# Kernel optimization log

Measured on AMD Instinct MI355X. Metric: run time of the kernel, lower is better.

Reference implementation:

```python
import jax, jax.numpy as jnp
import numpy as np
from math import sqrt

# dims
B, H, P, N, D = 4, 8, 32, 32, 16   # batch, heads, n_patches, channels, patch_len
L = P * N                           # 1024 token positions
SEQ, PRED, WIN, E, NF = 512, 96, 10, 2, 6  # seq_len, pred_len, attention_window, e_layers, n_fore
EPS = float(np.finfo(np.float32).eps)      # torch RMSNorm default eps (finfo eps)


def setup_inputs() -> dict:
    key = jax.random.key(0)
    ks = jax.random.split(key, 8)
    return dict(
        tokens=jax.random.normal(ks[0], (B, H, L, D), jnp.float32),
        x_original=jax.random.normal(ks[1], (B, SEQ, N), jnp.float32),
        log_scales=jnp.full((E,), np.log(2.0), jnp.float32),
        attn_norm_w=jnp.ones((E, D), jnp.float32),
        conv_up_w=jax.random.normal(ks[2], (E, 2 * H, 1, 3), jnp.float32) * 0.1,
        conv_down_w=jax.random.normal(ks[3], (E, H, 2, 1), jnp.float32) * 0.1,
        ffn_norm_w=jnp.ones((E, D), jnp.float32),
        mix_w=jax.random.normal(ks[4], (1, H), jnp.float32) * 0.3,
        mix_b=jnp.zeros((1,), jnp.float32),
        fore_w=jax.random.normal(ks[5], (NF, P), jnp.float32) * 0.1,
        fore_b=jnp.zeros((NF,), jnp.float32),
    )


def _rms(x, w):
    # torch.nn.RMSNorm over last dim (patch_len)
    return x * jax.lax.rsqrt(jnp.mean(x * x, axis=-1, keepdims=True) + EPS) * w


def _mask():
    # pid repeated per-channel; True entries are masked out
    pid = jnp.repeat(jnp.arange(P), N)
    diff = pid[None, :] - pid[:, None]  # pid[key] - pid[query]
    return (diff <= 0) | (diff >= WIN)  # [L, L]


def _signed_attn(h, log_scale, mask):
    # scores: [B,H,L,L]; A = softmax(+s) - softmax(-s) with banded mask
    scores = jnp.einsum('bhld,bhmd->bhlm', h, h)
    scale = jnp.clip(jnp.exp(log_scale), 1.0, 30.0) / sqrt(D)
    pos = jnp.where(mask, -10000.0, scores)
    neg = jnp.where(mask, -10000.0, -scores)
    A = jax.nn.softmax(scale * pos, axis=-1) - jax.nn.softmax(scale * neg, axis=-1)
    return jnp.einsum('bhlm,bhmd->bhld', A, h)


def _conv_ffn(x, up_w, down_w, norm_w):
    # depthwise causal conv along patch time dim D; x: [B,H,L,D]
    r = x.transpose(0, 2, 1, 3).reshape(B * L, H, D)
    r = jnp.pad(r, ((0, 0), (0, 0), (2, 0)))  # causal left-pad (kernel_size-1)
    dn = ('NCH', 'OIH', 'NCH')
    r = jax.lax.conv_general_dilated(r, up_w, (1,), 'VALID', dimension_numbers=dn, feature_group_count=H)
    r = jax.nn.gelu(r, approximate=False)
    r = jax.lax.conv_general_dilated(r, down_w, (1,), 'VALID', dimension_numbers=dn, feature_group_count=H)
    r = r.reshape(B, L, H, D).transpose(0, 2, 1, 3)
    return _rms(x + r, norm_w)


def reference(tokens, x_original, log_scales, attn_norm_w, conv_up_w, conv_down_w,
              ffn_norm_w, mix_w, mix_b, fore_w, fore_b):
    mask = _mask()
    h = tokens
    for l in range(E):
        h = _rms(h + _signed_attn(h, log_scales[l], mask), attn_norm_w[l])
        h = _conv_ffn(h, conv_up_w[l], conv_down_w[l], ffn_norm_w[l])
    # aggregate heads -> forecast
    h = h.reshape(B, H, P, N, D).transpose(0, 3, 4, 2, 1)       # (B,N,D,P,H)
    h = jnp.einsum('bndph,h->bndp', h, mix_w[0]) + mix_b[0]      # channel_mixing
    f = jnp.einsum('bndp,fp->bndf', h, fore_w) + fore_b          # fore_projection
    f = f.reshape(B, N, D * NF)[:, :, -PRED:]                    # flatten + tail slice
    forecast = f.transpose(0, 2, 1)                              # (B,pred_len,N)
    return forecast, x_original
```

## Files before the change

kernel.cpp:

```cpp
#include <hip/hip_runtime.h>
#include <hip/hip_bf16.h>
#include <math.h>

#define BB 4
#define HH 8
#define PP 32
#define NN 32
#define DD 16
#define LL 1024
#define WINW 10
#define NFF 6
#define PREDL 96
#define SEQL 512
#define EPSF 1.1920928955078125e-07f
#define KROW 24
#define KTS 296
#define PROW 40
#define XROW 20

typedef __attribute__((ext_vector_type(8))) short bf16x8;
typedef __attribute__((ext_vector_type(4))) float f32x4;

__device__ inline short f2bs(float f) {
    __hip_bfloat16 h = __float2bfloat16(f);
    return *reinterpret_cast<short*>(&h);
}

__global__ __launch_bounds__(128) void layer_kernel(
    const float* __restrict__ hin, float* __restrict__ hout,
    const float* __restrict__ log_scales, const float* __restrict__ attn_norm,
    const float* __restrict__ up_w, const float* __restrict__ down_w,
    const float* __restrict__ ffn_norm, int layer)
{
    __shared__ short hK[9 * 32 * KROW];
    __shared__ short VT[16 * KTS];
    __shared__ short Pp[2][16 * PROW];
    __shared__ short Pn[2][16 * PROW];
    __shared__ float xls[32 * XROW];

    int blk = blockIdx.x;
    int bh  = blk >> 5;
    int hh  = bh & 7;
    int p0  = blk & 31;
    int nstage = min(9, (PP - 1) - p0);

    int tid  = threadIdx.x;
    int wid  = tid >> 6;
    int lane = tid & 63;
    int quad = lane >> 4, n16 = lane & 15;

    {
        const float4* src = (const float4*)(hin + ((size_t)bh * LL + (p0 + 1) * NN) * DD);
        if (nstage == 9) {
            #pragma unroll
            for (int k = 0; k < 9; ++k) {
                int i = tid + k * 128;
                int row = i >> 2, j = i & 3;
                float4 v = src[i];
                short s0 = f2bs(v.x), s1 = f2bs(v.y), s2 = f2bs(v.z), s3 = f2bs(v.w);
                unsigned long long u =
                      (unsigned long long)(unsigned short)s0
                    | ((unsigned long long)(unsigned short)s1 << 16)
                    | ((unsigned long long)(unsigned short)s2 << 32)
                    | ((unsigned long long)(unsigned short)s3 << 48);
                *(unsigned long long*)&hK[row * KROW + j * 4] = u;
                int d0 = j * 4;
                VT[(d0 + 0) * KTS + row] = s0;
                VT[(d0 + 1) * KTS + row] = s1;
                VT[(d0 + 2) * KTS + row] = s2;
                VT[(d0 + 3) * KTS + row] = s3;
            }
        } else {
            int nf4 = nstage * 128;
            for (int i = tid; i < nf4; i += 128) {
                int row = i >> 2, j = i & 3;
                float4 v = src[i];
                short s0 = f2bs(v.x), s1 = f2bs(v.y), s2 = f2bs(v.z), s3 = f2bs(v.w);
                unsigned long long u =
                      (unsigned long long)(unsigned short)s0
                    | ((unsigned long long)(unsigned short)s1 << 16)
                    | ((unsigned long long)(unsigned short)s2 << 32)
                    | ((unsigned long long)(unsigned short)s3 << 48);
                *(unsigned long long*)&hK[row * KROW + j * 4] = u;
                int d0 = j * 4;
                VT[(d0 + 0) * KTS + row] = s0;
                VT[(d0 + 1) * KTS + row] = s1;
                VT[(d0 + 2) * KTS + row] = s2;
                VT[(d0 + 3) * KTS + row] = s3;
            }
        }
    }

    bf16x8 Aq;
    #pragma unroll
    for (int j = 0; j < 8; ++j) Aq[j] = 0;
    if (quad < 2) {
        const float* qp = hin + ((size_t)bh * LL + p0 * NN + wid * 16 + n16) * DD + quad * 8;
        #pragma unroll
        for (int j = 0; j < 8; ++j) Aq[j] = f2bs(qp[j]);
    }
    float rs[4];
    #pragma unroll
    for (int r = 0; r < 4; ++r)
        rs[r] = hin[((size_t)bh * LL + p0 * NN + wid * 16 + quad * 4 + r) * DD + n16];

    float sc = fminf(fmaxf(__expf(log_scales[layer]), 1.0f), 30.0f) * 0.25f;

    __syncthreads();

    f32x4 Op, On;
    Op[0] = Op[1] = Op[2] = Op[3] = 0.f;
    On[0] = On[1] = On[2] = On[3] = 0.f;
    float lpp[4] = {0.f, 0.f, 0.f, 0.f}, lnn[4] = {0.f, 0.f, 0.f, 0.f};
    short* myPp = Pp[wid];
    short* myPn = Pn[wid];

    for (int c = 0; c < nstage; ++c) {
        int kb = c * 32;
        #pragma unroll
        for (int kt = 0; kt < 2; ++kt) {
            bf16x8 Bk;
            #pragma unroll
            for (int j = 0; j < 8; ++j) Bk[j] = 0;
            if (quad < 2)
                Bk = *(const bf16x8*)&hK[(kb + kt * 16 + n16) * KROW + quad * 8];
            f32x4 z; z[0] = z[1] = z[2] = z[3] = 0.f;
            f32x4 S = __builtin_amdgcn_mfma_f32_16x16x32_bf16(Aq, Bk, z, 0, 0, 0);
            #pragma unroll
            for (int r = 0; r < 4; ++r) {
                float s  = S[r];
                float ep = __expf(sc * s);
                float en = __expf(-sc * s);
                lpp[r] += ep; lnn[r] += en;
                int pr = quad * 4 + r, pc = kt * 16 + n16;
                myPp[pr * PROW + pc] = f2bs(ep);
                myPn[pr * PROW + pc] = f2bs(en);
            }
        }
        bf16x8 Bv = *(const bf16x8*)&VT[n16 * KTS + kb + quad * 8];
        bf16x8 Ap = *(const bf16x8*)&myPp[n16 * PROW + quad * 8];
        bf16x8 An = *(const bf16x8*)&myPn[n16 * PROW + quad * 8];
        Op = __builtin_amdgcn_mfma_f32_16x16x32_bf16(Ap, Bv, Op, 0, 0, 0);
        On = __builtin_amdgcn_mfma_f32_16x16x32_bf16(An, Bv, On, 0, 0, 0);
    }

    #pragma unroll
    for (int r = 0; r < 4; ++r) {
        float a = lpp[r], b = lnn[r];
        a += __shfl_xor(a, 1); a += __shfl_xor(a, 2); a += __shfl_xor(a, 4); a += __shfl_xor(a, 8);
        b += __shfl_xor(b, 1); b += __shfl_xor(b, 2); b += __shfl_xor(b, 4); b += __shfl_xor(b, 8);
        lpp[r] = a; lnn[r] = b;
    }

    #pragma unroll
    for (int r = 0; r < 4; ++r) {
        float lp = lpp[r], ln = lnn[r];
        float rl = (lp > 0.f) ? (1.0f / lp) : 0.f;
        float rn = (ln > 0.f) ? (1.0f / ln) : 0.f;
        float v  = rs[r] + Op[r] * rl - On[r] * rn;
        float ss = v * v;
        ss += __shfl_xor(ss, 1); ss += __shfl_xor(ss, 2);
        ss += __shfl_xor(ss, 4); ss += __shfl_xor(ss, 8);
        float rr = rsqrtf(ss * (1.0f / 16.0f) + EPSF);
        xls[(wid * 16 + quad * 4 + r) * XROW + n16] = v * rr * attn_norm[layer * DD + n16];
    }

    if (lane < 16) {
        int q = wid * 16 + lane;
        float x[16];
        #pragma unroll
        for (int j = 0; j < 4; ++j) {
            float4 v = *(const float4*)&xls[q * XROW + j * 4];
            x[j*4+0] = v.x; x[j*4+1] = v.y; x[j*4+2] = v.z; x[j*4+3] = v.w;
        }

        const float* uw = up_w + (size_t)(layer * 2 * HH + 2 * hh) * 3;
        float w00 = uw[0], w01 = uw[1], w02 = uw[2];
        float w10 = uw[3], w11 = uw[4], w12 = uw[5];
        const float* dw = down_w + (size_t)(layer * HH + hh) * 2;
        float dc0 = dw[0], dc1 = dw[1];

        float v[16], ss = 0.f;
        #pragma unroll
        for (int i = 0; i < 16; ++i) {
            float xm2 = (i >= 2) ? x[i - 2] : 0.f;
            float xm1 = (i >= 1) ? x[i - 1] : 0.f;
            float u0 = w00 * xm2 + w01 * xm1 + w02 * x[i];
            float u1 = w10 * xm2 + w11 * xm1 + w12 * x[i];
            float g0 = 0.5f * u0 * (1.0f + erff(u0 * 0.7071067811865475f));
            float g1 = 0.5f * u1 * (1.0f + erff(u1 * 0.7071067811865475f));
            float vv = x[i] + dc0 * g0 + dc1 * g1;
            v[i] = vv; ss += vv * vv;
        }
        float r2 = rsqrtf(ss * (1.0f / 16.0f) + EPSF);
        float* op = hout + ((size_t)bh * LL + p0 * NN + q) * DD;
        #pragma unroll
        for (int i = 0; i < 16; ++i) op[i] = v[i] * r2 * ffn_norm[layer * DD + i];
    }
}

__global__ void tail_kernel(const float* __restrict__ h, const float* __restrict__ mw_,
                            const float* __restrict__ mb_, const float* __restrict__ fw_,
                            const float* __restrict__ fb_, const float* __restrict__ x,
                            float* __restrict__ out)
{
    int t = blockIdx.x * 256 + threadIdx.x;
    if (t < BB * DD * NFF * NN) {
        int n = t & 31;
        int r = t >> 5;
        int fi = r % NFF; r /= NFF;
        int d = r & 15;
        int b = r >> 4;

        float mw[8];
        #pragma unroll
        for (int k = 0; k < 8; ++k) mw[k] = mw_[k];
        float mb = mb_[0];

        float acc = fb_[fi];
        for (int p = 0; p < PP; ++p) {
            float m = mb;
            #pragma unroll
            for (int k = 0; k < 8; ++k)
                m += h[(size_t)(((b * HH + k) * LL) + p * NN + n) * DD + d] * mw[k];
            acc += m * fw_[fi * PP + p];
        }
        out[t] = acc;
    } else {
        int u4 = t - BB * DD * NFF * NN;
        if (u4 < BB * SEQL * NN / 4) {
            const float4* x4 = (const float4*)x;
            float4* o4 = (float4*)(out + BB * PREDL * NN);
            o4[u4] = x4[u4];
        }
    }
}

static int find_by_size(const int* s, int n, int want, int occurrence) {
    int seen = 0;
    for (int i = 0; i < n; ++i)
        if (s[i] == want) { if (seen == occurrence) return i; ++seen; }
    return -1;
}

extern "C" void kernel_launch(void* const* d_in, const int* in_sizes, int n_in,
                              void* d_out, int out_size, void* d_ws, size_t ws_size,
                              hipStream_t stream) {
    int it  = find_by_size(in_sizes, n_in, 524288, 0);
    int ix  = find_by_size(in_sizes, n_in, 65536, 0);
    int ils = find_by_size(in_sizes, n_in, 2, 0);
    int ian = find_by_size(in_sizes, n_in, 32, 0);
    int icu = find_by_size(in_sizes, n_in, 96, 0);
    int icd = find_by_size(in_sizes, n_in, 32, 1);
    int ifn = find_by_size(in_sizes, n_in, 32, 2);
    int imw = find_by_size(in_sizes, n_in, 8, 0);
    int imb = find_by_size(in_sizes, n_in, 1, 0);
    int ifw = find_by_size(in_sizes, n_in, 192, 0);
    int ifb = find_by_size(in_sizes, n_in, 6, 0);
    if (it < 0 || ix < 0 || ils < 0 || ian < 0 || icu < 0 || icd < 0 ||
        ifn < 0 || imw < 0 || imb < 0 || ifw < 0 || ifb < 0) {
        it = 0; ix = 1; ils = 2; ian = 3; icu = 4; icd = 5; ifn = 6;
        imw = 7; imb = 8; ifw = 9; ifb = 10;
    }

    const float* tokens     = (const float*)d_in[it];
    const float* x_orig     = (const float*)d_in[ix];
    const float* log_scales = (const float*)d_in[ils];
    const float* attn_norm  = (const float*)d_in[ian];
    const float* up_w       = (const float*)d_in[icu];
    const float* down_w     = (const float*)d_in[icd];
    const float* ffn_norm   = (const float*)d_in[ifn];
    const float* mix_w      = (const float*)d_in[imw];
    const float* mix_b      = (const float*)d_in[imb];
    const float* fore_w     = (const float*)d_in[ifw];
    const float* fore_b     = (const float*)d_in[ifb];
    float* out = (float*)d_out;

    const size_t NH = (size_t)BB * HH * LL * DD;
    float* hA = (float*)d_ws;
    float* hB = hA + NH;

    layer_kernel<<<1024, 128, 0, stream>>>(tokens, hA, log_scales, attn_norm,
                                           up_w, down_w, ffn_norm, 0);
    layer_kernel<<<1024, 128, 0, stream>>>(hA, hB, log_scales, attn_norm,
                                           up_w, down_w, ffn_norm, 1);
    const int tail_threads = BB * DD * NFF * NN + BB * SEQL * NN / 4;
    tail_kernel<<<(tail_threads + 255) / 256, 256, 0, stream>>>(
        hB, mix_w, mix_b, fore_w, fore_b, x_orig, out);
}
```

Baseline: 132.2 us.

## Split key chunks across two wave pairs and read keys directly from global

Doubles the block to 256 threads so that two pairs of waves each process alternating key chunks of the banded attention. Partial outputs and softmax denominators from the second pair are reduced through shared memory before the epilogue. The K staging buffer is removed, and keys are loaded from global memory and converted to bf16 in registers. This adds parallelism per block and cuts LDS use, at the cost of an extra barrier, an idle epilogue for half the waves, and redundant global key loads.

After: 137.6 us. 4.1% more time.

```diff
diff --git a/kernel.cpp b/kernel.cpp
--- a/kernel.cpp
+++ b/kernel.cpp
@@ -13,7 +13,6 @@
 #define PREDL 96
 #define SEQL 512
 #define EPSF 1.1920928955078125e-07f
-#define KROW 24
 #define KTS 296
 #define PROW 40
 #define XROW 20
@@ -26,17 +25,18 @@
     return *reinterpret_cast<short*>(&h);
 }
 
-__global__ __launch_bounds__(128) void layer_kernel(
+__global__ __launch_bounds__(256) void layer_kernel(
     const float* __restrict__ hin, float* __restrict__ hout,
     const float* __restrict__ log_scales, const float* __restrict__ attn_norm,
     const float* __restrict__ up_w, const float* __restrict__ down_w,
     const float* __restrict__ ffn_norm, int layer)
 {
-    __shared__ short hK[9 * 32 * KROW];
     __shared__ short VT[16 * KTS];
-    __shared__ short Pp[2][16 * PROW];
-    __shared__ short Pn[2][16 * PROW];
+    __shared__ short Pp[4][16 * PROW];
+    __shared__ short Pn[4][16 * PROW];
     __shared__ float xls[32 * XROW];
+    __shared__ float xchg[2][64][8];
+    __shared__ float lsm[2][4][4][2];
 
     int blk = blockIdx.x;
     int bh  = blk >> 5;
@@ -46,48 +46,25 @@
 
     int tid  = threadIdx.x;
     int wid  = tid >> 6;
+    int qt   = wid & 1;
+    int ch   = wid >> 1;
     int lane = tid & 63;
     int quad = lane >> 4, n16 = lane & 15;
 
+    const float* hbase = hin + (size_t)bh * LL * DD;
+    const float* kglob = hbase + (size_t)(p0 + 1) * NN * DD;
+
     {
-        const float4* src = (const float4*)(hin + ((size_t)bh * LL + (p0 + 1) * NN) * DD);
-        if (nstage == 9) {
-            #pragma unroll
-            for (int k = 0; k < 9; ++k) {
-                int i = tid + k * 128;
-                int row = i >> 2, j = i & 3;
-                float4 v = src[i];
-                short s0 = f2bs(v.x), s1 = f2bs(v.y), s2 = f2bs(v.z), s3 = f2bs(v.w);
-                unsigned long long u =
-                      (unsigned long long)(unsigned short)s0
-                    | ((unsigned long long)(unsigned short)s1 << 16)
-                    | ((unsigned long long)(unsigned short)s2 << 32)
-                    | ((unsigned long long)(unsigned short)s3 << 48);
-                *(unsigned long long*)&hK[row * KROW + j * 4] = u;
-                int d0 = j * 4;
-                VT[(d0 + 0) * KTS + row] = s0;
-                VT[(d0 + 1) * KTS + row] = s1;
-                VT[(d0 + 2) * KTS + row] = s2;
-                VT[(d0 + 3) * KTS + row] = s3;
-            }
-        } else {
-            int nf4 = nstage * 128;
-            for (int i = tid; i < nf4; i += 128) {
-                int row = i >> 2, j = i & 3;
-                float4 v = src[i];
-                short s0 = f2bs(v.x), s1 = f2bs(v.y), s2 = f2bs(v.z), s3 = f2bs(v.w);
-                unsigned long long u =
-                      (unsigned long long)(unsigned short)s0
-                    | ((unsigned long long)(unsigned short)s1 << 16)
-                    | ((unsigned long long)(unsigned short)s2 << 32)
-                    | ((unsigned long long)(unsigned short)s3 << 48);
-                *(unsigned long long*)&hK[row * KROW + j * 4] = u;
-                int d0 = j * 4;
-                VT[(d0 + 0) * KTS + row] = s0;
-                VT[(d0 + 1) * KTS + row] = s1;
-                VT[(d0 + 2) * KTS + row] = s2;
-                VT[(d0 + 3) * KTS + row] = s3;
-            }
+        const float4* src = (const float4*)kglob;
+        int nf4 = nstage * 128;
+        for (int i = tid; i < nf4; i += 256) {
+            int row = i >> 2, j = i & 3;
+            float4 v = src[i];
+            int d0 = j * 4;
+            VT[(d0 + 0) * KTS + row] = f2bs(v.x);
+            VT[(d0 + 1) * KTS + row] = f2bs(v.y);
+            VT[(d0 + 2) * KTS + row] = f2bs(v.z);
+            VT[(d0 + 3) * KTS + row] = f2bs(v.w);
         }
     }
 
@@ -95,14 +72,14 @@
     #pragma unroll
     for (int j = 0; j < 8; ++j) Aq[j] = 0;
     if (quad < 2) {
-        const float* qp = hin + ((size_t)bh * LL + p0 * NN + wid * 16 + n16) * DD + quad * 8;
+        const float* qp = hbase + (size_t)(p0 * NN + qt * 16 + n16) * DD + quad * 8;
         #pragma unroll
         for (int j = 0; j < 8; ++j) Aq[j] = f2bs(qp[j]);
     }
     float rs[4];
     #pragma unroll
     for (int r = 0; r < 4; ++r)
-        rs[r] = hin[((size_t)bh * LL + p0 * NN + wid * 16 + quad * 4 + r) * DD + n16];
+        rs[r] = hbase[(size_t)(p0 * NN + qt * 16 + quad * 4 + r) * DD + n16];
 
     float sc = fminf(fmaxf(__expf(log_scales[layer]), 1.0f), 30.0f) * 0.25f;
 
@@ -115,15 +92,20 @@
     short* myPp = Pp[wid];
     short* myPn = Pn[wid];
 
-    for (int c = 0; c < nstage; ++c) {
+    for (int c = ch; c < nstage; c += 2) {
         int kb = c * 32;
         #pragma unroll
         for (int kt = 0; kt < 2; ++kt) {
             bf16x8 Bk;
             #pragma unroll
             for (int j = 0; j < 8; ++j) Bk[j] = 0;
-            if (quad < 2)
-                Bk = *(const bf16x8*)&hK[(kb + kt * 16 + n16) * KROW + quad * 8];
+            if (quad < 2) {
+                const float* kp = kglob + (size_t)(kb + kt * 16 + n16) * DD + quad * 8;
+                float4 v0 = *(const float4*)kp;
+                float4 v1 = *(const float4*)(kp + 4);
+                Bk[0] = f2bs(v0.x); Bk[1] = f2bs(v0.y); Bk[2] = f2bs(v0.z); Bk[3] = f2bs(v0.w);
+                Bk[4] = f2bs(v1.x); Bk[5] = f2bs(v1.y); Bk[6] = f2bs(v1.z); Bk[7] = f2bs(v1.w);
+            }
             f32x4 z; z[0] = z[1] = z[2] = z[3] = 0.f;
             f32x4 S = __builtin_amdgcn_mfma_f32_16x16x32_bf16(Aq, Bk, z, 0, 0, 0);
             #pragma unroll
@@ -152,50 +134,76 @@
         lpp[r] = a; lnn[r] = b;
     }
 
-    #pragma unroll
-    for (int r = 0; r < 4; ++r) {
-        float lp = lpp[r], ln = lnn[r];
-        float rl = (lp > 0.f) ? (1.0f / lp) : 0.f;
-        float rn = (ln > 0.f) ? (1.0f / ln) : 0.f;
-        float v  = rs[r] + Op[r] * rl - On[r] * rn;
-        float ss = v * v;
-        ss += __shfl_xor(ss, 1); ss += __shfl_xor(ss, 2);
-        ss += __shfl_xor(ss, 4); ss += __shfl_xor(ss, 8);
-        float rr = rsqrtf(ss * (1.0f / 16.0f) + EPSF);
-        xls[(wid * 16 + quad * 4 + r) * XROW + n16] = v * rr * attn_norm[layer * DD + n16];
-    }
-
-    if (lane < 16) {
-        int q = wid * 16 + lane;
-        float x[16];
-        #pragma unroll
-        for (int j = 0; j < 4; ++j) {
-            float4 v = *(const float4*)&xls[q * XROW + j * 4];
-            x[j*4+0] = v.x; x[j*4+1] = v.y; x[j*4+2] = v.z; x[j*4+3] = v.w;
-        }
-
-        const float* uw = up_w + (size_t)(layer * 2 * HH + 2 * hh) * 3;
-        float w00 = uw[0], w01 = uw[1], w02 = uw[2];
-        float w10 = uw[3], w11 = uw[4], w12 = uw[5];
-        const float* dw = down_w + (size_t)(layer * HH + hh) * 2;
-        float dc0 = dw[0], dc1 = dw[1];
-
-        float v[16], ss = 0.f;
-        #pragma unroll
-        for (int i = 0; i < 16; ++i) {
-            float xm2 = (i >= 2) ? x[i - 2] : 0.f;
-            float xm1 = (i >= 1) ? x[i - 1] : 0.f;
-            float u0 = w00 * xm2 + w01 * xm1 + w02 * x[i];
-            float u1 = w10 * xm2 + w11 * xm1 + w12 * x[i];
-            float g0 = 0.5f * u0 * (1.0f + erff(u0 * 0.7071067811865475f));
-            float g1 = 0.5f * u1 * (1.0f + erff(u1 * 0.7071067811865475f));
-            float vv = x[i] + dc0 * g0 + dc1 * g1;
-            v[i] = vv; ss += vv * vv;
-        }
-        float r2 = rsqrtf(ss * (1.0f / 16.0f) + EPSF);
-        float* op = hout + ((size_t)bh * LL + p0 * NN + q) * DD;
-        #pragma unroll
-        for (int i = 0; i < 16; ++i) op[i] = v[i] * r2 * ffn_norm[layer * DD + i];
+    if (ch == 1) {
+        #pragma unroll
+        for (int r = 0; r < 4; ++r) {
+            xchg[qt][lane][r]     = Op[r];
+            xchg[qt][lane][r + 4] = On[r];
+        }
+        if (n16 == 0) {
+            #pragma unroll
+            for (int r = 0; r < 4; ++r) {
+                lsm[qt][quad][r][0] = lpp[r];
+                lsm[qt][quad][r][1] = lnn[r];
+            }
+        }
+    }
+    __syncthreads();
+
+    if (ch == 0) {
+        #pragma unroll
+        for (int r = 0; r < 4; ++r) {
+            Op[r]  += xchg[qt][lane][r];
+            On[r]  += xchg[qt][lane][r + 4];
+            lpp[r] += lsm[qt][quad][r][0];
+            lnn[r] += lsm[qt][quad][r][1];
+        }
+
+        #pragma unroll
+        for (int r = 0; r < 4; ++r) {
+            float lp = lpp[r], ln = lnn[r];
+            float rl = (lp > 0.f) ? (1.0f / lp) : 0.f;
+            float rn = (ln > 0.f) ? (1.0f / ln) : 0.f;
+            float v  = rs[r] + Op[r] * rl - On[r] * rn;
+            float ss = v * v;
+            ss += __shfl_xor(ss, 1); ss += __shfl_xor(ss, 2);
+            ss += __shfl_xor(ss, 4); ss += __shfl_xor(ss, 8);
+            float rr = rsqrtf(ss * (1.0f / 16.0f) + EPSF);
+            xls[(qt * 16 + quad * 4 + r) * XROW + n16] = v * rr * attn_norm[layer * DD + n16];
+        }
+
+        if (lane < 16) {
+            int q = qt * 16 + lane;
+            float x[16];
+            #pragma unroll
+            for (int j = 0; j < 4; ++j) {
+                float4 v = *(const float4*)&xls[q * XROW + j * 4];
+                x[j*4+0] = v.x; x[j*4+1] = v.y; x[j*4+2] = v.z; x[j*4+3] = v.w;
+            }
+
+            const float* uw = up_w + (size_t)(layer * 2 * HH + 2 * hh) * 3;
+            float w00 = uw[0], w01 = uw[1], w02 = uw[2];
+            float w10 = uw[3], w11 = uw[4], w12 = uw[5];
+            const float* dw = down_w + (size_t)(layer * HH + hh) * 2;
+            float dc0 = dw[0], dc1 = dw[1];
+
+            float v[16], ss = 0.f;
+            #pragma unroll
+            for (int i = 0; i < 16; ++i) {
+                float xm2 = (i >= 2) ? x[i - 2] : 0.f;
+                float xm1 = (i >= 1) ? x[i - 1] : 0.f;
+                float u0 = w00 * xm2 + w01 * xm1 + w02 * x[i];
+                float u1 = w10 * xm2 + w11 * xm1 + w12 * x[i];
+                float g0 = 0.5f * u0 * (1.0f + erff(u0 * 0.7071067811865475f));
+                float g1 = 0.5f * u1 * (1.0f + erff(u1 * 0.7071067811865475f));
+                float vv = x[i] + dc0 * g0 + dc1 * g1;
+                v[i] = vv; ss += vv * vv;
+            }
+            float r2 = rsqrtf(ss * (1.0f / 16.0f) + EPSF);
+            float* op = hout + ((size_t)bh * LL + p0 * NN + q) * DD;
+            #pragma unroll
+            for (int i = 0; i < 16; ++i) op[i] = v[i] * r2 * ffn_norm[layer * DD + i];
+        }
     }
 }
 
@@ -280,9 +288,9 @@
     float* hA = (float*)d_ws;
     float* hB = hA + NH;
 
-    layer_kernel<<<1024, 128, 0, stream>>>(tokens, hA, log_scales, attn_norm,
+    layer_kernel<<<1024, 256, 0, stream>>>(tokens, hA, log_scales, attn_norm,
                                            up_w, down_w, ffn_norm, 0);
-    layer_kernel<<<1024, 128, 0, stream>>>(hA, hB, log_scales, attn_norm,
+    layer_kernel<<<1024, 256, 0, stream>>>(hA, hB, log_scales, attn_norm,
                                            up_w, down_w, ffn_norm, 1);
     const int tail_threads = BB * DD * NFF * NN + BB * SEQL * NN / 4;
     tail_kernel<<<(tail_threads + 255) / 256, 256, 0, stream>>>(
```

## Fuse both layers and tail into one cooperative kernel with grid syncs

Applied to the files above, without the earlier changes.

Merges the two layer launches and the tail launch into a single cooperative kernel of 1024 blocks, using grid-wide syncs between stages. The aim is to remove kernel launch gaps and inter-kernel drain and fill. Shared memory moves into a struct passed by pointer. If the cooperative launch fails it falls back to the old three-launch path, and grid.sync adds barrier cost.

Result: slower. 337.6 us (+155.4%).

```diff
diff --git a/kernel.cpp b/kernel.cpp
--- a/kernel.cpp
+++ b/kernel.cpp
@@ -1,6 +1,9 @@
 #include <hip/hip_runtime.h>
 #include <hip/hip_bf16.h>
+#include <hip/hip_cooperative_groups.h>
 #include <math.h>
+
+namespace cg = cooperative_groups;
 
 #define BB 4
 #define HH 8
@@ -26,18 +29,21 @@
     return *reinterpret_cast<short*>(&h);
 }
 
-__global__ __launch_bounds__(128) void layer_kernel(
+struct __align__(16) LayerSmem {
+    short hK[9 * 32 * KROW];
+    short VT[16 * KTS];
+    short Pp[2][16 * PROW];
+    short Pn[2][16 * PROW];
+    float xls[32 * XROW];
+};
+
+__device__ __forceinline__ void do_layer(
+    LayerSmem* sm,
     const float* __restrict__ hin, float* __restrict__ hout,
     const float* __restrict__ log_scales, const float* __restrict__ attn_norm,
     const float* __restrict__ up_w, const float* __restrict__ down_w,
     const float* __restrict__ ffn_norm, int layer)
 {
-    __shared__ short hK[9 * 32 * KROW];
-    __shared__ short VT[16 * KTS];
-    __shared__ short Pp[2][16 * PROW];
-    __shared__ short Pn[2][16 * PROW];
-    __shared__ float xls[32 * XROW];
-
     int blk = blockIdx.x;
     int bh  = blk >> 5;
     int hh  = bh & 7;
@@ -63,12 +69,12 @@
                     | ((unsigned long long)(unsigned short)s1 << 16)
                     | ((unsigned long long)(unsigned short)s2 << 32)
                     | ((unsigned long long)(unsigned short)s3 << 48);
-                *(unsigned long long*)&hK[row * KROW + j * 4] = u;
+                *(unsigned long long*)&sm->hK[row * KROW + j * 4] = u;
                 int d0 = j * 4;
-                VT[(d0 + 0) * KTS + row] = s0;
-                VT[(d0 + 1) * KTS + row] = s1;
-                VT[(d0 + 2) * KTS + row] = s2;
-                VT[(d0 + 3) * KTS + row] = s3;
+                sm->VT[(d0 + 0) * KTS + row] = s0;
+                sm->VT[(d0 + 1) * KTS + row] = s1;
+                sm->VT[(d0 + 2) * KTS + row] = s2;
+                sm->VT[(d0 + 3) * KTS + row] = s3;
             }
         } else {
             int nf4 = nstage * 128;
@@ -81,12 +87,12 @@
                     | ((unsigned long long)(unsigned short)s1 << 16)
                     | ((unsigned long long)(unsigned short)s2 << 32)
                     | ((unsigned long long)(unsigned short)s3 << 48);
-                *(unsigned long long*)&hK[row * KROW + j * 4] = u;
+                *(unsigned long long*)&sm->hK[row * KROW + j * 4] = u;
                 int d0 = j * 4;
-                VT[(d0 + 0) * KTS + row] = s0;
-                VT[(d0 + 1) * KTS + row] = s1;
-                VT[(d0 + 2) * KTS + row] = s2;
-                VT[(d0 + 3) * KTS + row] = s3;
+                sm->VT[(d0 + 0) * KTS + row] = s0;
+                sm->VT[(d0 + 1) * KTS + row] = s1;
+                sm->VT[(d0 + 2) * KTS + row] = s2;
+                sm->VT[(d0 + 3) * KTS + row] = s3;
             }
         }
     }
@@ -112,8 +118,8 @@
     Op[0] = Op[1] = Op[2] = Op[3] = 0.f;
     On[0] = On[1] = On[2] = On[3] = 0.f;
     float lpp[4] = {0.f, 0.f, 0.f, 0.f}, lnn[4] = {0.f, 0.f, 0.f, 0.f};
-    short* myPp = Pp[wid];
-    short* myPn = Pn[wid];
+    short* myPp = sm->Pp[wid];
+    short* myPn = sm->Pn[wid];
 
     for (int c = 0; c < nstage; ++c) {
         int kb = c * 32;
@@ -123,7 +129,7 @@
             #pragma unroll
             for (int j = 0; j < 8; ++j) Bk[j] = 0;
             if (quad < 2)
-                Bk = *(const bf16x8*)&hK[(kb + kt * 16 + n16) * KROW + quad * 8];
+                Bk = *(const bf16x8*)&sm->hK[(kb + kt * 16 + n16) * KROW + quad * 8];
             f32x4 z; z[0] = z[1] = z[2] = z[3] = 0.f;
             f32x4 S = __builtin_amdgcn_mfma_f32_16x16x32_bf16(Aq, Bk, z, 0, 0, 0);
             #pragma unroll
@@ -137,7 +143,7 @@
                 myPn[pr * PROW + pc] = f2bs(en);
             }
         }
-        bf16x8 Bv = *(const bf16x8*)&VT[n16 * KTS + kb + quad * 8];
+        bf16x8 Bv = *(const bf16x8*)&sm->VT[n16 * KTS + kb + quad * 8];
         bf16x8 Ap = *(const bf16x8*)&myPp[n16 * PROW + quad * 8];
         bf16x8 An = *(const bf16x8*)&myPn[n16 * PROW + quad * 8];
         Op = __builtin_amdgcn_mfma_f32_16x16x32_bf16(Ap, Bv, Op, 0, 0, 0);
@@ -162,7 +168,7 @@
         ss += __shfl_xor(ss, 1); ss += __shfl_xor(ss, 2);
         ss += __shfl_xor(ss, 4); ss += __shfl_xor(ss, 8);
         float rr = rsqrtf(ss * (1.0f / 16.0f) + EPSF);
-        xls[(wid * 16 + quad * 4 + r) * XROW + n16] = v * rr * attn_norm[layer * DD + n16];
+        sm->xls[(wid * 16 + quad * 4 + r) * XROW + n16] = v * rr * attn_norm[layer * DD + n16];
     }
 
     if (lane < 16) {
@@ -170,7 +176,7 @@
         float x[16];
         #pragma unroll
         for (int j = 0; j < 4; ++j) {
-            float4 v = *(const float4*)&xls[q * XROW + j * 4];
+            float4 v = *(const float4*)&sm->xls[q * XROW + j * 4];
             x[j*4+0] = v.x; x[j*4+1] = v.y; x[j*4+2] = v.z; x[j*4+3] = v.w;
         }
 
@@ -199,12 +205,12 @@
     }
 }
 
-__global__ void tail_kernel(const float* __restrict__ h, const float* __restrict__ mw_,
-                            const float* __restrict__ mb_, const float* __restrict__ fw_,
-                            const float* __restrict__ fb_, const float* __restrict__ x,
-                            float* __restrict__ out)
-{
-    int t = blockIdx.x * 256 + threadIdx.x;
+__device__ __forceinline__ void do_tail(
+    int t, const float* __restrict__ h, const float* __restrict__ mw_,
+    const float* __restrict__ mb_, const float* __restrict__ fw_,
+    const float* __restrict__ fb_, const float* __restrict__ x,
+    float* __restrict__ out)
+{
     if (t < BB * DD * NFF * NN) {
         int n = t & 31;
         int r = t >> 5;
@@ -234,6 +240,44 @@
             o4[u4] = x4[u4];
         }
     }
+}
+
+__global__ __launch_bounds__(128) void mega_kernel(
+    const float* __restrict__ tokens, float* __restrict__ hA, float* __restrict__ hB,
+    const float* __restrict__ log_scales, const float* __restrict__ attn_norm,
+    const float* __restrict__ up_w, const float* __restrict__ down_w,
+    const float* __restrict__ ffn_norm, const float* __restrict__ mw_,
+    const float* __restrict__ mb_, const float* __restrict__ fw_,
+    const float* __restrict__ fb_, const float* __restrict__ x,
+    float* __restrict__ out)
+{
+    __shared__ LayerSmem sm;
+    cg::grid_group grid = cg::this_grid();
+
+    do_layer(&sm, tokens, hA, log_scales, attn_norm, up_w, down_w, ffn_norm, 0);
+    grid.sync();
+    do_layer(&sm, hA, hB, log_scales, attn_norm, up_w, down_w, ffn_norm, 1);
+    grid.sync();
+
+    do_tail(blockIdx.x * 128 + threadIdx.x, hB, mw_, mb_, fw_, fb_, x, out);
+}
+
+__global__ __launch_bounds__(128) void layer_kernel(
+    const float* __restrict__ hin, float* __restrict__ hout,
+    const float* __restrict__ log_scales, const float* __restrict__ attn_norm,
+    const float* __restrict__ up_w, const float* __restrict__ down_w,
+    const float* __restrict__ ffn_norm, int layer)
+{
+    __shared__ LayerSmem sm;
+    do_layer(&sm, hin, hout, log_scales, attn_norm, up_w, down_w, ffn_norm, layer);
+}
+
+__global__ void tail_kernel(const float* __restrict__ h, const float* __restrict__ mw_,
+                            const float* __restrict__ mb_, const float* __restrict__ fw_,
+                            const float* __restrict__ fb_, const float* __restrict__ x,
+                            float* __restrict__ out)
+{
+    do_tail(blockIdx.x * 256 + threadIdx.x, h, mw_, mb_, fw_, fb_, x, out);
 }
 
 static int find_by_size(const int* s, int n, int want, int occurrence) {
@@ -280,11 +324,22 @@
     float* hA = (float*)d_ws;
     float* hB = hA + NH;
 
-    layer_kernel<<<1024, 128, 0, stream>>>(tokens, hA, log_scales, attn_norm,
-                                           up_w, down_w, ffn_norm, 0);
-    layer_kernel<<<1024, 128, 0, stream>>>(hA, hB, log_scales, attn_norm,
-                                           up_w, down_w, ffn_norm, 1);
-    const int tail_threads = BB * DD * NFF * NN + BB * SEQL * NN / 4;
-    tail_kernel<<<(tail_threads + 255) / 256, 256, 0, stream>>>(
-        hB, mix_w, mix_b, fore_w, fore_b, x_orig, out);
-}
+    void* args[] = {
+        (void*)&tokens, (void*)&hA, (void*)&hB, (void*)&log_scales,
+        (void*)&attn_norm, (void*)&up_w, (void*)&down_w, (void*)&ffn_norm,
+        (void*)&mix_w, (void*)&mix_b, (void*)&fore_w, (void*)&fore_b,
+        (void*)&x_orig, (void*)&out
+    };
+    hipError_t err = hipLaunchCooperativeKernel((void*)mega_kernel, dim3(1024),
+                                                dim3(128), args, 0, stream);
+    if (err != hipSuccess) {
+        (void)hipGetLastError();
+        layer_kernel<<<1024, 128, 0, stream>>>(tokens, hA, log_scales, attn_norm,
+                                               up_w, down_w, ffn_norm, 0);
+        layer_kernel<<<1024, 128, 0, stream>>>(hA, hB, log_scales, attn_norm,
+                                               up_w, down_w, ffn_norm, 1);
+        const int tail_threads = BB * DD * NFF * NN + BB * SEQL * NN / 4;
+        tail_kernel<<<(tail_threads + 255) / 256, 256, 0, stream>>>(
+            hB, mix_w, mix_b, fore_w, fore_b, x_orig, out);
+    }
+}
```

## Read K and V operands directly from global memory instead of LDS staging

Applied to the files above, without the earlier changes.

Removes the shared-memory staging of the key tile and the transposed value tile, along with the block-wide barrier that followed it. Each wave now loads its K fragments as float4 pairs and its V fragments as strided scalar loads from global memory inside the stage loop, converting them to bf16 in registers. This drops the LDS footprint and the upfront cooperative copy, which may raise occupancy. The cost is more global/L2 traffic, since both waves fetch the same keys, and uncoalesced strided V loads on the critical path of each stage.

Measured after the change: 134.9 us. 1.02x slower.

```diff
diff --git a/kernel.cpp b/kernel.cpp
--- a/kernel.cpp
+++ b/kernel.cpp
@@ -13,8 +13,6 @@
 #define PREDL 96
 #define SEQL 512
 #define EPSF 1.1920928955078125e-07f
-#define KROW 24
-#define KTS 296
 #define PROW 40
 #define XROW 20
 
@@ -32,8 +30,6 @@
     const float* __restrict__ up_w, const float* __restrict__ down_w,
     const float* __restrict__ ffn_norm, int layer)
 {
-    __shared__ short hK[9 * 32 * KROW];
-    __shared__ short VT[16 * KTS];
     __shared__ short Pp[2][16 * PROW];
     __shared__ short Pn[2][16 * PROW];
     __shared__ float xls[32 * XROW];
@@ -49,64 +45,23 @@
     int lane = tid & 63;
     int quad = lane >> 4, n16 = lane & 15;
 
-    {
-        const float4* src = (const float4*)(hin + ((size_t)bh * LL + (p0 + 1) * NN) * DD);
-        if (nstage == 9) {
-            #pragma unroll
-            for (int k = 0; k < 9; ++k) {
-                int i = tid + k * 128;
-                int row = i >> 2, j = i & 3;
-                float4 v = src[i];
-                short s0 = f2bs(v.x), s1 = f2bs(v.y), s2 = f2bs(v.z), s3 = f2bs(v.w);
-                unsigned long long u =
-                      (unsigned long long)(unsigned short)s0
-                    | ((unsigned long long)(unsigned short)s1 << 16)
-                    | ((unsigned long long)(unsigned short)s2 << 32)
-                    | ((unsigned long long)(unsigned short)s3 << 48);
-                *(unsigned long long*)&hK[row * KROW + j * 4] = u;
-                int d0 = j * 4;
-                VT[(d0 + 0) * KTS + row] = s0;
-                VT[(d0 + 1) * KTS + row] = s1;
-                VT[(d0 + 2) * KTS + row] = s2;
-                VT[(d0 + 3) * KTS + row] = s3;
-            }
-        } else {
-            int nf4 = nstage * 128;
-            for (int i = tid; i < nf4; i += 128) {
-                int row = i >> 2, j = i & 3;
-                float4 v = src[i];
-                short s0 = f2bs(v.x), s1 = f2bs(v.y), s2 = f2bs(v.z), s3 = f2bs(v.w);
-                unsigned long long u =
-                      (unsigned long long)(unsigned short)s0
-                    | ((unsigned long long)(unsigned short)s1 << 16)
-                    | ((unsigned long long)(unsigned short)s2 << 32)
-                    | ((unsigned long long)(unsigned short)s3 << 48);
-                *(unsigned long long*)&hK[row * KROW + j * 4] = u;
-                int d0 = j * 4;
-                VT[(d0 + 0) * KTS + row] = s0;
-                VT[(d0 + 1) * KTS + row] = s1;
-                VT[(d0 + 2) * KTS + row] = s2;
-                VT[(d0 + 3) * KTS + row] = s3;
-            }
-        }
-    }
+    const float* hbase = hin + (size_t)bh * LL * DD;
+    const float* kglob = hbase + (size_t)(p0 + 1) * NN * DD;
 
     bf16x8 Aq;
     #pragma unroll
     for (int j = 0; j < 8; ++j) Aq[j] = 0;
     if (quad < 2) {
-        const float* qp = hin + ((size_t)bh * LL + p0 * NN + wid * 16 + n16) * DD + quad * 8;
+        const float* qp = hbase + (size_t)(p0 * NN + wid * 16 + n16) * DD + quad * 8;
         #pragma unroll
         for (int j = 0; j < 8; ++j) Aq[j] = f2bs(qp[j]);
     }
     float rs[4];
     #pragma unroll
     for (int r = 0; r < 4; ++r)
-        rs[r] = hin[((size_t)bh * LL + p0 * NN + wid * 16 + quad * 4 + r) * DD + n16];
+        rs[r] = hbase[(size_t)(p0 * NN + wid * 16 + quad * 4 + r) * DD + n16];
 
     float sc = fminf(fmaxf(__expf(log_scales[layer]), 1.0f), 30.0f) * 0.25f;
-
-    __syncthreads();
 
     f32x4 Op, On;
     Op[0] = Op[1] = Op[2] = Op[3] = 0.f;
@@ -117,13 +72,26 @@
 
     for (int c = 0; c < nstage; ++c) {
         int kb = c * 32;
+
+        bf16x8 Bvc;
+        {
+            const float* vp = kglob + (size_t)(kb + quad * 8) * DD + n16;
+            #pragma unroll
+            for (int j = 0; j < 8; ++j) Bvc[j] = f2bs(vp[j * DD]);
+        }
+
         #pragma unroll
         for (int kt = 0; kt < 2; ++kt) {
             bf16x8 Bk;
             #pragma unroll
             for (int j = 0; j < 8; ++j) Bk[j] = 0;
-            if (quad < 2)
-                Bk = *(const bf16x8*)&hK[(kb + kt * 16 + n16) * KROW + quad * 8];
+            if (quad < 2) {
+                const float* kp = kglob + (size_t)(kb + kt * 16 + n16) * DD + quad * 8;
+                float4 v0 = *(const float4*)kp;
+                float4 v1 = *(const float4*)(kp + 4);
+                Bk[0] = f2bs(v0.x); Bk[1] = f2bs(v0.y); Bk[2] = f2bs(v0.z); Bk[3] = f2bs(v0.w);
+                Bk[4] = f2bs(v1.x); Bk[5] = f2bs(v1.y); Bk[6] = f2bs(v1.z); Bk[7] = f2bs(v1.w);
+            }
             f32x4 z; z[0] = z[1] = z[2] = z[3] = 0.f;
             f32x4 S = __builtin_amdgcn_mfma_f32_16x16x32_bf16(Aq, Bk, z, 0, 0, 0);
             #pragma unroll
@@ -137,11 +105,10 @@
                 myPn[pr * PROW + pc] = f2bs(en);
             }
         }
-        bf16x8 Bv = *(const bf16x8*)&VT[n16 * KTS + kb + quad * 8];
         bf16x8 Ap = *(const bf16x8*)&myPp[n16 * PROW + quad * 8];
         bf16x8 An = *(const bf16x8*)&myPn[n16 * PROW + quad * 8];
-        Op = __builtin_amdgcn_mfma_f32_16x16x32_bf16(Ap, Bv, Op, 0, 0, 0);
-        On = __builtin_amdgcn_mfma_f32_16x16x32_bf16(An, Bv, On, 0, 0, 0);
+        Op = __builtin_amdgcn_mfma_f32_16x16x32_bf16(Ap, Bvc, Op, 0, 0, 0);
+        On = __builtin_amdgcn_mfma_f32_16x16x32_bf16(An, Bvc, On, 0, 0, 0);
     }
 
     #pragma unroll
```
